# Optimization experiments

Hardware: AMD Instinct MI355X
Metric: run time of the kernel (lower is better)

The kernel has to match this reference:

```python
import jax, jax.numpy as jnp
import numpy as np

PSI = 0.001  # convex-combination reconditioning strength
C, N, B = 4, 64, 2048


def _symmap(A, f, psi):
    # recondition via convex combination with identity, then apply f to the spectrum
    if psi > 0:
        A = (1.0 - psi) * A + psi * jnp.eye(A.shape[-1], dtype=A.dtype)
    L, Q = jnp.linalg.eigh(A)
    # Q diag(f(L)) Q^T
    return jnp.einsum('...ik,...k,...jk->...ij', Q, f(L), Q)


def setup_inputs() -> dict:
    key = jax.random.key(0)
    k1, k2 = jax.random.split(key)
    A = jax.random.normal(k1, (B, N, N), dtype=jnp.float32)
    inp = A @ A.swapaxes(-1, -2) / N + 0.1 * jnp.eye(N, dtype=jnp.float32)  # SPD [B,N,N]
    W = jax.random.normal(k2, (C, N, N), dtype=jnp.float32)
    weight = W @ W.swapaxes(-1, -2)  # module init: weight = W W^T, [C,N,N]
    return {'input': inp, 'weight': weight}


def reference(input, weight):
    # Omega^{-1/2} for each of the C tangency points
    ref_sri = _symmap(weight, lambda x: 1.0 / jnp.sqrt(x), PSI)  # [C,N,N]
    # congruence: Omega^{-1/2} Theta Omega^{-1/2}, broadcast over channels -> [B,C,N,N]
    cong = ref_sri @ input[..., None, :, :] @ ref_sri
    cong = 0.5 * (cong + cong.swapaxes(-1, -2))  # resymmetrize for eigh
    # matrix logarithm -> tangent-space vector field [B,C,N,N]
    return _symmap(cong, jnp.log, PSI)
```

## Files before the change

### kernel.cpp

```cpp
#include <hip/hip_runtime.h>
#include <math.h>

#define N 64
typedef float f32x2 __attribute__((ext_vector_type(2)));

__device__ __forceinline__ float bperm(int byteaddr, float v) {
    return __int_as_float(__builtin_amdgcn_ds_bpermute(byteaddr, __float_as_int(v)));
}
__device__ __forceinline__ float getrow(const f32x2 (&a)[N / 2], int i) {
    return (i & 1) ? a[i >> 1].y : a[i >> 1].x;
}
__device__ __forceinline__ void setrow(f32x2 (&a)[N / 2], int i, float v) {
    if (i & 1) a[i >> 1].y = v; else a[i >> 1].x = v;
}

__device__ __forceinline__ void transpose64(f32x2 (&a)[N / 2], int lane) {
#pragma unroll
    for (int b = 1; b < N; b <<= 1) {
        bool upper = (lane & b) != 0;
#pragma unroll
        for (int i = 0; i < N; ++i) {
            if ((i & b) == 0) {
                float lo = getrow(a, i), hi = getrow(a, i | b);
                float send = upper ? lo : hi;
                float recv = __shfl_xor(send, b, 64);
                setrow(a, i, upper ? recv : lo);
                setrow(a, i | b, upper ? hi : recv);
            }
        }
    }
}

__device__ __forceinline__ float norm2_64(const f32x2 (&g)[N / 2]) {
    f32x2 a = {0.f, 0.f}, b = {0.f, 0.f};
#pragma unroll
    for (int i = 0; i < N / 2; i += 2) {
        a = g[i] * g[i] + a;
        b = g[i + 1] * g[i + 1] + b;
    }
    f32x2 s = a + b;
    return s.x + s.y;
}

__device__ __forceinline__ float jacobi_onesided(f32x2 (&g)[N / 2], int lane, int max_sweeps) {
#pragma clang loop unroll(disable)
    for (int s = 0; s < max_sweeps; ++s) {
        float d = norm2_64(g);
        int anybad = 0;
#pragma clang loop unroll(disable)
        for (int m = 1; m < N; ++m) {
            int paddr = (lane ^ m) << 2;
            f32x2 t[N / 2];
#pragma unroll
            for (int i = 0; i < N / 2; ++i) {
                t[i].x = bperm(paddr, g[i].x);
                t[i].y = bperm(paddr, g[i].y);
            }
            f32x2 oa = {0.f, 0.f}, ob = {0.f, 0.f};
#pragma unroll
            for (int i = 0; i < N / 2; i += 2) {
                oa = g[i] * t[i] + oa;
                ob = g[i + 1] * t[i + 1] + ob;
            }
            f32x2 os = oa + ob;
            float o = os.x + os.y;
            float doth = bperm(paddr, d);
            bool is_lo = lane < (lane ^ m);
            float dp = is_lo ? d : doth;
            float dq = is_lo ? doth : d;
            anybad |= (o * o > 1e-11f * dp * dq) ? 1 : 0;
            bool skip = (o * o) <= (1e-24f * dp * dq);
            float osafe = skip ? 1.0f : o;
            float theta = (dq - dp) / (2.0f * osafe);
            float tt = -copysignf(1.0f, theta) /
                       (fabsf(theta) + sqrtf(fmaf(theta, theta, 1.0f)));
            float c = rsqrtf(fmaf(tt, tt, 1.0f));
            float sv = tt * c;
            c = skip ? 1.0f : c;
            sv = skip ? 0.0f : sv;
            float c2 = c * c, s2 = sv * sv, cso = 2.0f * c * sv * o;
            d = is_lo ? fmaf(c2, dp, fmaf(s2, dq, cso))
                      : fmaf(s2, dp, fmaf(c2, dq, -cso));
            d = fmaxf(d, 1e-30f);
            float ss = is_lo ? sv : -sv;
            f32x2 cv = {c, c}, sv2 = {ss, ss};
#pragma unroll
            for (int i = 0; i < N / 2; ++i)
                g[i] = sv2 * t[i] + cv * g[i];
        }
        if (!__any(anybad)) break;
    }
    return norm2_64(g);
}

__device__ __forceinline__ void spectral_recon_store(f32x2 (&g)[N / 2], float coef,
                                                     int lane, float* __restrict__ outp) {
    f32x2 rowg[N / 2];
#pragma unroll
    for (int i = 0; i < N / 2; ++i) rowg[i] = g[i];
    transpose64(rowg, lane);
#pragma unroll
    for (int k = 0; k < N; ++k) {
        float ck = bperm(k << 2, coef);
        setrow(rowg, k, getrow(rowg, k) * ck);
    }
#pragma unroll
    for (int base = 0; base < N; base += 16) {
        f32x2 acc[8];
#pragma unroll
        for (int j = 0; j < 8; ++j) { acc[j].x = 0.f; acc[j].y = 0.f; }
#pragma unroll
        for (int k = 0; k < N; ++k) {
            float w = getrow(rowg, k);
            f32x2 wv = {w, w};
            int kaddr = k << 2;
#pragma unroll
            for (int j = 0; j < 8; ++j) {
                f32x2 mv;
                mv.x = bperm(kaddr, g[base / 2 + j].x);
                mv.y = bperm(kaddr, g[base / 2 + j].y);
                acc[j] = mv * wv + acc[j];
            }
        }
#pragma unroll
        for (int j = 0; j < 8; ++j) {
            outp[(base + 2 * j) * N + lane]     = acc[j].x;
            outp[(base + 2 * j + 1) * N + lane] = acc[j].y;
        }
    }
}

__global__ __launch_bounds__(64) __attribute__((amdgpu_waves_per_eu(1)))
void prep_R(const float* __restrict__ wgt, float* __restrict__ Rws) {
    int c = blockIdx.x;
    int lane = threadIdx.x;
    const float* W = wgt + c * N * N;
    f32x2 g[N / 2];
#pragma unroll
    for (int i = 0; i < N; ++i)
        setrow(g, i, 0.999f * W[i * N + lane] + ((i == lane) ? 0.001f : 0.0f));
    float d = jacobi_onesided(g, lane, 15);
    float coef = sqrtf(rsqrtf(d)) / d;
    spectral_recon_store(g, coef, lane, Rws + c * N * N);
}

__global__ __launch_bounds__(64) __attribute__((amdgpu_waves_per_eu(1)))
void tangent_log(const float* __restrict__ inp, const float* __restrict__ Rws,
                 float* __restrict__ out) {
    int bid = blockIdx.x;
    int b = bid >> 2;
    int c = bid & 3;
    int lane = threadIdx.x;
    const float* Th = inp + (size_t)b * (N * N);
    const float* Rc = Rws + c * (N * N);

    f32x2 r[N / 2];
#pragma unroll
    for (int k = 0; k < N; ++k) setrow(r, k, Rc[k * N + lane]);

    f32x2 u[N / 2];
#pragma unroll
    for (int i = 0; i < N / 2; ++i) { u[i].x = 0.f; u[i].y = 0.f; }
#pragma unroll
    for (int k = 0; k < N; ++k) {
        const float4* row = (const float4*)(Th + k * N);
        float rk = getrow(r, k);
        f32x2 rv = {rk, rk};
#pragma unroll
        for (int q = 0; q < N / 4; ++q) {
            float4 v = row[q];
            f32x2 v0 = {v.x, v.y}, v1 = {v.z, v.w};
            u[2 * q]     = v0 * rv + u[2 * q];
            u[2 * q + 1] = v1 * rv + u[2 * q + 1];
        }
    }

    f32x2 g[N / 2];
#pragma unroll
    for (int i = 0; i < N / 2; ++i) { g[i].x = 0.f; g[i].y = 0.f; }
#pragma unroll
    for (int k = 0; k < N; ++k) {
        const float4* row = (const float4*)(Rc + k * N);
        float uk = getrow(u, k);
        f32x2 uv = {uk, uk};
#pragma unroll
        for (int q = 0; q < N / 4; ++q) {
            float4 v = row[q];
            f32x2 v0 = {v.x, v.y}, v1 = {v.z, v.w};
            g[2 * q]     = v0 * uv + g[2 * q];
            g[2 * q + 1] = v1 * uv + g[2 * q + 1];
        }
    }

    {
        f32x2 tr[N / 2];
#pragma unroll
        for (int i = 0; i < N / 2; ++i) tr[i] = g[i];
        transpose64(tr, lane);
        f32x2 h = {0.5f, 0.5f};
#pragma unroll
        for (int i = 0; i < N / 2; ++i) g[i] = h * (g[i] + tr[i]);
    }

#pragma unroll
    for (int i = 0; i < N; ++i)
        setrow(g, i, 0.999f * getrow(g, i) + ((i == lane) ? 0.001f : 0.0f));

    float d = jacobi_onesided(g, lane, 15);
    float coef = 0.5f * logf(d) / d;
    spectral_recon_store(g, coef, lane, out + (size_t)bid * (N * N));
}

extern "C" void kernel_launch(void* const* d_in, const int* in_sizes, int n_in,
                              void* d_out, int out_size, void* d_ws, size_t ws_size,
                              hipStream_t stream) {
    const float* inp = (const float*)d_in[0];
    const float* wgt = (const float*)d_in[1];
    float* out = (float*)d_out;
    float* Rws = (float*)d_ws;

    int B = in_sizes[0] / (N * N);
    int C = in_sizes[1] / (N * N);

    hipLaunchKernelGGL(prep_R, dim3(C), dim3(64), 0, stream, wgt, Rws);
    hipLaunchKernelGGL(tangent_log, dim3(B * C), dim3(64), 0, stream, inp, Rws, out);
}
```

Measured before the change: 5.501 ms.

## Split each matrix's Jacobi eigensolve across two waves with LDS reductions

Each 64x64 matrix now uses a 128-thread block instead of one wave. Each wave holds half the rows, so per-lane register state is halved and occupancy rises. Column-pair dot products and norms are reduced across the two waves through shared memory, with a barrier per rotation step. Rotation rounds where no lane exceeds the threshold are skipped wave-wide. The shuffle-based transposes and reconstruction are replaced by LDS-staged matrix transposes and products. This adds a __syncthreads per Jacobi step, and the wave-uniform skip via `continue` must stay consistent across both waves, which puts barrier divergence at risk.

```diff
diff --git a/kernel.cpp b/kernel.cpp
--- a/kernel.cpp
+++ b/kernel.cpp
@@ -2,213 +2,203 @@
 #include <math.h>
 
 #define N 64
+#define LSTR 66
 typedef float f32x2 __attribute__((ext_vector_type(2)));
+
+struct Smem {
+    float mat[N * LSTR];
+    float nbuf[2 * N];
+    float obuf[2][2 * N];
+    float coefbuf[N];
+};
 
 __device__ __forceinline__ float bperm(int byteaddr, float v) {
     return __int_as_float(__builtin_amdgcn_ds_bpermute(byteaddr, __float_as_int(v)));
 }
-__device__ __forceinline__ float getrow(const f32x2 (&a)[N / 2], int i) {
-    return (i & 1) ? a[i >> 1].y : a[i >> 1].x;
-}
-__device__ __forceinline__ void setrow(f32x2 (&a)[N / 2], int i, float v) {
-    if (i & 1) a[i >> 1].y = v; else a[i >> 1].x = v;
-}
-
-__device__ __forceinline__ void transpose64(f32x2 (&a)[N / 2], int lane) {
-#pragma unroll
-    for (int b = 1; b < N; b <<= 1) {
-        bool upper = (lane & b) != 0;
-#pragma unroll
-        for (int i = 0; i < N; ++i) {
-            if ((i & b) == 0) {
-                float lo = getrow(a, i), hi = getrow(a, i | b);
-                float send = upper ? lo : hi;
-                float recv = __shfl_xor(send, b, 64);
-                setrow(a, i, upper ? recv : lo);
-                setrow(a, i | b, upper ? hi : recv);
-            }
-        }
-    }
-}
-
-__device__ __forceinline__ float norm2_64(const f32x2 (&g)[N / 2]) {
+
+__device__ __forceinline__ float norm2half(const f32x2 (&g)[16]) {
     f32x2 a = {0.f, 0.f}, b = {0.f, 0.f};
 #pragma unroll
-    for (int i = 0; i < N / 2; i += 2) {
-        a = g[i] * g[i] + a;
-        b = g[i + 1] * g[i + 1] + b;
-    }
+    for (int i = 0; i < 16; i += 2) { a = g[i] * g[i] + a; b = g[i + 1] * g[i + 1] + b; }
     f32x2 s = a + b;
     return s.x + s.y;
 }
 
-__device__ __forceinline__ float jacobi_onesided(f32x2 (&g)[N / 2], int lane, int max_sweeps) {
+__device__ float jacobi_split(f32x2 (&g)[16], int lane, int wid, Smem& S, int max_sweeps) {
+    float d = 0.f;
 #pragma clang loop unroll(disable)
     for (int s = 0; s < max_sweeps; ++s) {
-        float d = norm2_64(g);
+        S.nbuf[wid * N + lane] = norm2half(g);
+        __syncthreads();
+        d = S.nbuf[lane] + S.nbuf[N + lane];
+        __syncthreads();
         int anybad = 0;
 #pragma clang loop unroll(disable)
         for (int m = 1; m < N; ++m) {
             int paddr = (lane ^ m) << 2;
-            f32x2 t[N / 2];
-#pragma unroll
-            for (int i = 0; i < N / 2; ++i) {
+            f32x2 t[16];
+#pragma unroll
+            for (int i = 0; i < 16; ++i) {
                 t[i].x = bperm(paddr, g[i].x);
                 t[i].y = bperm(paddr, g[i].y);
             }
             f32x2 oa = {0.f, 0.f}, ob = {0.f, 0.f};
 #pragma unroll
-            for (int i = 0; i < N / 2; i += 2) {
-                oa = g[i] * t[i] + oa;
-                ob = g[i + 1] * t[i + 1] + ob;
-            }
+            for (int i = 0; i < 16; i += 2) { oa = g[i] * t[i] + oa; ob = g[i + 1] * t[i + 1] + ob; }
             f32x2 os = oa + ob;
-            float o = os.x + os.y;
             float doth = bperm(paddr, d);
+            int p = m & 1;
+            S.obuf[p][wid * N + lane] = os.x + os.y;
+            __syncthreads();
+            float o = S.obuf[p][lane] + S.obuf[p][N + lane];
             bool is_lo = lane < (lane ^ m);
             float dp = is_lo ? d : doth;
             float dq = is_lo ? doth : d;
-            anybad |= (o * o > 1e-11f * dp * dq) ? 1 : 0;
+            int roundbad = __any(o * o > 1e-11f * dp * dq);
+            anybad |= roundbad;
+            if (!roundbad) continue;
             bool skip = (o * o) <= (1e-24f * dp * dq);
             float osafe = skip ? 1.0f : o;
             float theta = (dq - dp) / (2.0f * osafe);
             float tt = -copysignf(1.0f, theta) /
                        (fabsf(theta) + sqrtf(fmaf(theta, theta, 1.0f)));
-            float c = rsqrtf(fmaf(tt, tt, 1.0f));
-            float sv = tt * c;
-            c = skip ? 1.0f : c;
+            float cc = rsqrtf(fmaf(tt, tt, 1.0f));
+            float sv = tt * cc;
+            cc = skip ? 1.0f : cc;
             sv = skip ? 0.0f : sv;
-            float c2 = c * c, s2 = sv * sv, cso = 2.0f * c * sv * o;
+            float c2 = cc * cc, s2 = sv * sv, cso = 2.0f * cc * sv * o;
             d = is_lo ? fmaf(c2, dp, fmaf(s2, dq, cso))
                       : fmaf(s2, dp, fmaf(c2, dq, -cso));
             d = fmaxf(d, 1e-30f);
             float ss = is_lo ? sv : -sv;
-            f32x2 cv = {c, c}, sv2 = {ss, ss};
-#pragma unroll
-            for (int i = 0; i < N / 2; ++i)
-                g[i] = sv2 * t[i] + cv * g[i];
+            f32x2 cv = {cc, cc}, sv2 = {ss, ss};
+#pragma unroll
+            for (int i = 0; i < 16; ++i) g[i] = sv2 * t[i] + cv * g[i];
         }
         if (!__any(anybad)) break;
     }
-    return norm2_64(g);
-}
-
-__device__ __forceinline__ void spectral_recon_store(f32x2 (&g)[N / 2], float coef,
-                                                     int lane, float* __restrict__ outp) {
-    f32x2 rowg[N / 2];
-#pragma unroll
-    for (int i = 0; i < N / 2; ++i) rowg[i] = g[i];
-    transpose64(rowg, lane);
-#pragma unroll
+    S.nbuf[wid * N + lane] = norm2half(g);
+    __syncthreads();
+    d = S.nbuf[lane] + S.nbuf[N + lane];
+    __syncthreads();
+    return d;
+}
+
+__device__ void recon_store(const f32x2 (&g)[16], float coef, int lane, int wid,
+                            Smem& S, float* __restrict__ outp) {
+    int row0 = wid * 32;
+    if (wid == 0) S.coefbuf[lane] = coef;
+#pragma unroll
+    for (int i = 0; i < 16; ++i)
+        *(f32x2*)&S.mat[lane * LSTR + row0 + 2 * i] = g[i];
+    __syncthreads();
+    f32x2 acc[16];
+#pragma unroll
+    for (int i = 0; i < 16; ++i) acc[i] = (f32x2){0.f, 0.f};
+#pragma clang loop unroll(disable)
     for (int k = 0; k < N; ++k) {
-        float ck = bperm(k << 2, coef);
-        setrow(rowg, k, getrow(rowg, k) * ck);
-    }
-#pragma unroll
-    for (int base = 0; base < N; base += 16) {
-        f32x2 acc[8];
-#pragma unroll
-        for (int j = 0; j < 8; ++j) { acc[j].x = 0.f; acc[j].y = 0.f; }
-#pragma unroll
-        for (int k = 0; k < N; ++k) {
-            float w = getrow(rowg, k);
-            f32x2 wv = {w, w};
-            int kaddr = k << 2;
-#pragma unroll
-            for (int j = 0; j < 8; ++j) {
-                f32x2 mv;
-                mv.x = bperm(kaddr, g[base / 2 + j].x);
-                mv.y = bperm(kaddr, g[base / 2 + j].y);
-                acc[j] = mv * wv + acc[j];
-            }
+        float wk = S.coefbuf[k] * S.mat[k * LSTR + lane];
+        f32x2 wv = {wk, wk};
+        const f32x2* col = (const f32x2*)&S.mat[k * LSTR + row0];
+#pragma unroll
+        for (int i = 0; i < 16; ++i) acc[i] = col[i] * wv + acc[i];
+    }
+#pragma unroll
+    for (int i = 0; i < 16; ++i) {
+        outp[(row0 + 2 * i) * N + lane]     = acc[i].x;
+        outp[(row0 + 2 * i + 1) * N + lane] = acc[i].y;
+    }
+}
+
+__global__ __launch_bounds__(128, 4) void prep_R(const float* __restrict__ wgt,
+                                                 float* __restrict__ Rws) {
+    __shared__ Smem S;
+    int c = blockIdx.x;
+    int tid = threadIdx.x, wid = tid >> 6, lane = tid & 63;
+    int row0 = wid * 32;
+    const float* W = wgt + (size_t)c * (N * N);
+    f32x2 g[16];
+#pragma unroll
+    for (int i = 0; i < 16; ++i) {
+        g[i].x = 0.999f * W[(row0 + 2 * i) * N + lane]     + ((row0 + 2 * i)     == lane ? 0.001f : 0.f);
+        g[i].y = 0.999f * W[(row0 + 2 * i + 1) * N + lane] + ((row0 + 2 * i + 1) == lane ? 0.001f : 0.f);
+    }
+    float d = jacobi_split(g, lane, wid, S, 15);
+    float coef = sqrtf(rsqrtf(d)) / d;
+    recon_store(g, coef, lane, wid, S, Rws + (size_t)c * (N * N));
+}
+
+__global__ __launch_bounds__(128, 4) void tangent_log(const float* __restrict__ inp,
+                                                      const float* __restrict__ Rws,
+                                                      float* __restrict__ out) {
+    __shared__ Smem S;
+    int bid = blockIdx.x, b = bid >> 2, c = bid & 3;
+    int tid = threadIdx.x, wid = tid >> 6, lane = tid & 63;
+    int row0 = wid * 32;
+    const float* Th = inp + (size_t)b * (N * N);
+    const float* Rc = Rws + (size_t)c * (N * N);
+
+    f32x2 r[32];
+#pragma unroll
+    for (int k = 0; k < 32; ++k) {
+        r[k].x = Rc[(2 * k) * N + lane];
+        r[k].y = Rc[(2 * k + 1) * N + lane];
+    }
+#pragma clang loop unroll(disable)
+    for (int i = 0; i < 32; ++i) {
+        const float4* __restrict__ row = (const float4*)(Th + (size_t)(row0 + i) * N);
+        f32x2 a = {0.f, 0.f}, bacc = {0.f, 0.f};
+#pragma unroll
+        for (int q = 0; q < 16; q += 2) {
+            float4 v0 = row[q], v1 = row[q + 1];
+            a    = (f32x2){v0.x, v0.y} * r[2 * q]     + a;
+            a    = (f32x2){v0.z, v0.w} * r[2 * q + 1] + a;
+            bacc = (f32x2){v1.x, v1.y} * r[2 * q + 2] + bacc;
+            bacc = (f32x2){v1.z, v1.w} * r[2 * q + 3] + bacc;
         }
-#pragma unroll
-        for (int j = 0; j < 8; ++j) {
-            outp[(base + 2 * j) * N + lane]     = acc[j].x;
-            outp[(base + 2 * j + 1) * N + lane] = acc[j].y;
+        f32x2 sres = a + bacc;
+        S.mat[(row0 + i) * LSTR + lane] = sres.x + sres.y;
+    }
+    __syncthreads();
+    f32x2 ucol[32];
+#pragma unroll
+    for (int k = 0; k < 32; ++k) {
+        ucol[k].x = S.mat[(2 * k) * LSTR + lane];
+        ucol[k].y = S.mat[(2 * k + 1) * LSTR + lane];
+    }
+    __syncthreads();
+#pragma clang loop unroll(disable)
+    for (int i = 0; i < 32; ++i) {
+        const float4* __restrict__ row = (const float4*)(Rc + (size_t)(row0 + i) * N);
+        f32x2 a = {0.f, 0.f}, bacc = {0.f, 0.f};
+#pragma unroll
+        for (int q = 0; q < 16; q += 2) {
+            float4 v0 = row[q], v1 = row[q + 1];
+            a    = (f32x2){v0.x, v0.y} * ucol[2 * q]     + a;
+            a    = (f32x2){v0.z, v0.w} * ucol[2 * q + 1] + a;
+            bacc = (f32x2){v1.x, v1.y} * ucol[2 * q + 2] + bacc;
+            bacc = (f32x2){v1.z, v1.w} * ucol[2 * q + 3] + bacc;
         }
-    }
-}
-
-__global__ __launch_bounds__(64) __attribute__((amdgpu_waves_per_eu(1)))
-void prep_R(const float* __restrict__ wgt, float* __restrict__ Rws) {
-    int c = blockIdx.x;
-    int lane = threadIdx.x;
-    const float* W = wgt + c * N * N;
-    f32x2 g[N / 2];
-#pragma unroll
-    for (int i = 0; i < N; ++i)
-        setrow(g, i, 0.999f * W[i * N + lane] + ((i == lane) ? 0.001f : 0.0f));
-    float d = jacobi_onesided(g, lane, 15);
-    float coef = sqrtf(rsqrtf(d)) / d;
-    spectral_recon_store(g, coef, lane, Rws + c * N * N);
-}
-
-__global__ __launch_bounds__(64) __attribute__((amdgpu_waves_per_eu(1)))
-void tangent_log(const float* __restrict__ inp, const float* __restrict__ Rws,
-                 float* __restrict__ out) {
-    int bid = blockIdx.x;
-    int b = bid >> 2;
-    int c = bid & 3;
-    int lane = threadIdx.x;
-    const float* Th = inp + (size_t)b * (N * N);
-    const float* Rc = Rws + c * (N * N);
-
-    f32x2 r[N / 2];
-#pragma unroll
-    for (int k = 0; k < N; ++k) setrow(r, k, Rc[k * N + lane]);
-
-    f32x2 u[N / 2];
-#pragma unroll
-    for (int i = 0; i < N / 2; ++i) { u[i].x = 0.f; u[i].y = 0.f; }
-#pragma unroll
-    for (int k = 0; k < N; ++k) {
-        const float4* row = (const float4*)(Th + k * N);
-        float rk = getrow(r, k);
-        f32x2 rv = {rk, rk};
-#pragma unroll
-        for (int q = 0; q < N / 4; ++q) {
-            float4 v = row[q];
-            f32x2 v0 = {v.x, v.y}, v1 = {v.z, v.w};
-            u[2 * q]     = v0 * rv + u[2 * q];
-            u[2 * q + 1] = v1 * rv + u[2 * q + 1];
-        }
-    }
-
-    f32x2 g[N / 2];
-#pragma unroll
-    for (int i = 0; i < N / 2; ++i) { g[i].x = 0.f; g[i].y = 0.f; }
-#pragma unroll
-    for (int k = 0; k < N; ++k) {
-        const float4* row = (const float4*)(Rc + k * N);
-        float uk = getrow(u, k);
-        f32x2 uv = {uk, uk};
-#pragma unroll
-        for (int q = 0; q < N / 4; ++q) {
-            float4 v = row[q];
-            f32x2 v0 = {v.x, v.y}, v1 = {v.z, v.w};
-            g[2 * q]     = v0 * uv + g[2 * q];
-            g[2 * q + 1] = v1 * uv + g[2 * q + 1];
-        }
-    }
-
-    {
-        f32x2 tr[N / 2];
-#pragma unroll
-        for (int i = 0; i < N / 2; ++i) tr[i] = g[i];
-        transpose64(tr, lane);
+        f32x2 sres = a + bacc;
+        S.mat[(row0 + i) * LSTR + lane] = sres.x + sres.y;
+    }
+    __syncthreads();
+    f32x2 g[16];
+#pragma unroll
+    for (int i = 0; i < 16; ++i) {
+        f32x2 own;
+        own.x = S.mat[(row0 + 2 * i) * LSTR + lane];
+        own.y = S.mat[(row0 + 2 * i + 1) * LSTR + lane];
+        f32x2 tr = *(const f32x2*)&S.mat[lane * LSTR + row0 + 2 * i];
         f32x2 h = {0.5f, 0.5f};
-#pragma unroll
-        for (int i = 0; i < N / 2; ++i) g[i] = h * (g[i] + tr[i]);
-    }
-
-#pragma unroll
-    for (int i = 0; i < N; ++i)
-        setrow(g, i, 0.999f * getrow(g, i) + ((i == lane) ? 0.001f : 0.0f));
-
-    float d = jacobi_onesided(g, lane, 15);
+        g[i] = h * (own + tr);
+        g[i].x = 0.999f * g[i].x + ((row0 + 2 * i)     == lane ? 0.001f : 0.f);
+        g[i].y = 0.999f * g[i].y + ((row0 + 2 * i + 1) == lane ? 0.001f : 0.f);
+    }
+
+    float d = jacobi_split(g, lane, wid, S, 15);
     float coef = 0.5f * logf(d) / d;
-    spectral_recon_store(g, coef, lane, out + (size_t)bid * (N * N));
+    recon_store(g, coef, lane, wid, S, out + (size_t)bid * (N * N));
 }
 
 extern "C" void kernel_launch(void* const* d_in, const int* in_sizes, int n_in,
@@ -222,6 +212,6 @@
     int B = in_sizes[0] / (N * N);
     int C = in_sizes[1] / (N * N);
 
-    hipLaunchKernelGGL(prep_R, dim3(C), dim3(64), 0, stream, wgt, Rws);
-    hipLaunchKernelGGL(tangent_log, dim3(B * C), dim3(64), 0, stream, inp, Rws, out);
-}
+    hipLaunchKernelGGL(prep_R, dim3(C), dim3(128), 0, stream, wgt, Rws);
+    hipLaunchKernelGGL(tangent_log, dim3(B * C), dim3(128), 0, stream, inp, Rws, out);
+}
```

Result: slower. 5.919 ms (+7.6%).
